# Kernel tuning notes

Measured on AMD Instinct MI355X. Metric: run time of the kernel, lower is better.

## Reference

```python
import jax, jax.numpy as jnp
import numpy as np

N_NODES = 50000
N_EDGES = 800000
F_IN, F_HID, F_OUT = 128, 256, 64


def setup_inputs() -> dict:
    key = jax.random.key(0)
    ks = jax.random.split(key, 8)
    return {
        "x": jax.random.normal(ks[0], (N_NODES, F_IN), dtype=jnp.float32),
        "edge_index": jax.random.randint(ks[1], (2, N_EDGES), 0, N_NODES, dtype=jnp.int32),
        "W_l1": jax.random.normal(ks[2], (F_IN, F_HID), dtype=jnp.float32) * (1.0 / np.sqrt(F_IN)),
        "W_r1": jax.random.normal(ks[3], (F_IN, F_HID), dtype=jnp.float32) * (1.0 / np.sqrt(F_IN)),
        "b1": jnp.zeros((F_HID,), dtype=jnp.float32),
        "W_l2": jax.random.normal(ks[4], (F_HID, F_OUT), dtype=jnp.float32) * (1.0 / np.sqrt(F_HID)),
        "W_r2": jax.random.normal(ks[5], (F_HID, F_OUT), dtype=jnp.float32) * (1.0 / np.sqrt(F_HID)),
        "b2": jnp.zeros((F_OUT,), dtype=jnp.float32),
    }


def _sage_conv(x, src, dst, W_l, W_r, b):
    # PyG SAGEConv, mean aggregation:
    #   out = mean_{j in N(i)} x_j @ W_l + b + x_i @ W_r
    n = x.shape[0]
    msgs = x[src]                                              # [E, F] gather
    agg_sum = jax.ops.segment_sum(msgs, dst, num_segments=n)   # [N, F] scatter-add
    deg = jax.ops.segment_sum(jnp.ones_like(dst, dtype=x.dtype), dst, num_segments=n)
    agg = agg_sum / jnp.maximum(deg, 1.0)[:, None]             # isolated nodes -> 0
    return agg @ W_l + x @ W_r + b


def reference(x, edge_index, W_l1, W_r1, b1, W_l2, W_r2, b2):
    src, dst = edge_index[0], edge_index[1]
    # layer 1 + relu (dropout is identity in eval mode)
    h = jax.nn.relu(_sage_conv(x, src, dst, W_l1, W_r1, b1))
    # layer 2, multi_class=False -> sigmoid
    out = jax.nn.sigmoid(_sage_conv(h, src, dst, W_l2, W_r2, b2))
    return out
```

## Files before the change

kernel.cpp:

```cpp
#include <hip/hip_runtime.h>
#include <cstdint>
#include <cstddef>


#define N_NODES 50000
#define N_EDGES 800000
#define F_IN 128
#define F_HID 256
#define F_OUT 64
#define CAP 48
#define BINW 128

#define NBIN ((N_NODES + BINW - 1) / BINW)
#define EPB 4096
#define NBLK_A ((N_EDGES + EPB - 1) / EPB)
#define CHUNK 32

#define PREP_TOTAL (N_NODES * 64 + 256 * 256 + 128 * 256)
#define NBLK_PREP ((PREP_TOTAL + 255) / 256)

typedef __attribute__((ext_vector_type(8))) short bf16x8;
typedef __attribute__((ext_vector_type(4))) float f32x4;
typedef __attribute__((ext_vector_type(2))) float f32x2;

__device__ inline unsigned short f2bf(float f) {
    unsigned int u = __float_as_uint(f);
    u += 0x7fffu + ((u >> 16) & 1u);
    return (unsigned short)(u >> 16);
}
__device__ inline unsigned int pack_bf2(float lo, float hi) {
    return (unsigned int)f2bf(lo) | ((unsigned int)f2bf(hi) << 16);
}
__device__ inline float bf_lo(unsigned int u) { return __uint_as_float(u << 16); }
__device__ inline float bf_hi(unsigned int u) { return __uint_as_float(u & 0xffff0000u); }

__device__ inline void gload16(const short* g, short* l) {
    __builtin_amdgcn_global_load_lds(
        (const __attribute__((address_space(1))) void*)g,
        (__attribute__((address_space(3))) void*)l, 16, 0, 0);
}

__global__ __launch_bounds__(256) void binprep_kernel(
    const int* __restrict__ src, const int* __restrict__ dst, int* __restrict__ blkbincnt,
    unsigned int* __restrict__ chunks, const float* __restrict__ x,
    const float* __restrict__ Wl1, const float* __restrict__ Wr1, const float* __restrict__ Wl2,
    const float* __restrict__ Wr2, unsigned int* __restrict__ xbf,
    unsigned short* __restrict__ xq16, short* __restrict__ Bt1, short* __restrict__ Bt2) {
    __shared__ unsigned int ls[NBIN * CHUNK];
    __shared__ int hist[NBIN];
    const int bid = blockIdx.x;
    const int tid = threadIdx.x;
    if (bid < NBLK_A) {
        for (int i = tid; i < NBIN; i += 256) hist[i] = 0;
        __syncthreads();
        const int base = bid * EPB;
        const int nloc = min(EPB, N_EDGES - base);
        for (int j = tid; j < nloc; j += 256) {
            int e = base + j;
            int d = dst[e];
            int s = src[e];
            int bin = d >> 7;
            int p = atomicAdd(&hist[bin], 1);
            if (p < CHUNK)
                ls[bin * CHUNK + p] = ((unsigned int)(d & (BINW - 1)) << 16) | (unsigned int)s;
        }
        __syncthreads();
        for (int i = tid; i < NBIN; i += 256) blkbincnt[bid * NBIN + i] = hist[i];
        unsigned int* outp = &chunks[(size_t)bid * NBIN * CHUNK];
        for (int idx = tid; idx < NBIN * CHUNK; idx += 256) {
            int bin = idx >> 5, i = idx & 31;
            if (i < min(hist[bin], CHUNK)) outp[idx] = ls[idx];
        }
        return;
    }
    int i = (bid - NBLK_A) * 256 + tid;
    if (i < N_NODES * 64) {
        int row = i >> 6, c = i & 63;
        float2 f = *reinterpret_cast<const float2*>(&x[(size_t)row * F_IN + 2 * c]);
        xbf[(size_t)row * 64 + c] = pack_bf2(f.x, f.y);
        xq16[(size_t)row * 64 + c] =
            (unsigned short)(__builtin_amdgcn_cvt_pk_fp8_f32(f.x, f.y, 0, false) & 0xffff);
        return;
    }
    i -= N_NODES * 64;
    if (i < 256 * 256) {
        int k = i >> 8, n = i & 255;
        float v = (k < 128) ? Wl1[k * 256 + n] : Wr1[(k - 128) * 256 + n];
        Bt1[n * 256 + k] = (short)f2bf(v);
        return;
    }
    i -= 256 * 256;
    if (i < 128 * 256) {
        int k = i >> 7, n = i & 127;
        float v = (n < 64) ? Wl2[k * 64 + n] : Wr2[k * 64 + (n - 64)];
        Bt2[n * 256 + k] = (short)f2bf(v);
    }
}

__global__ __launch_bounds__(1024) void bpart_agg_kernel(const unsigned int* __restrict__ chunks,
                                                         const int* __restrict__ blkbincnt,
                                                         int* __restrict__ cnt,
                                                         unsigned short* __restrict__ slots,
                                                         const unsigned int* __restrict__ xq,
                                                         unsigned int* __restrict__ aggx) {
    __shared__ int cur[BINW];
    __shared__ unsigned short ls[BINW * CAP];
    __shared__ int ccnt[NBLK_A];
    const int bin = blockIdx.x;
    const int tid = threadIdx.x;
    if (tid < BINW) cur[tid] = 0;
    for (int i = tid; i < NBLK_A; i += 1024) ccnt[i] = min(blkbincnt[i * NBIN + bin], CHUNK);
    __syncthreads();
    for (int idx = tid; idx < NBLK_A * CHUNK; idx += 1024) {
        int blk = idx >> 5, i = idx & 31;
        if (i < ccnt[blk]) {
            unsigned int pk = chunks[((size_t)blk * NBIN + bin) * CHUNK + i];
            int dl = pk >> 16;
            int p = atomicAdd(&cur[dl], 1);
            if (p < CAP) ls[dl * CAP + p] = (unsigned short)(pk & 0xffffu);
        }
    }
    __syncthreads();
    if (tid < BINW) {
        int node = bin * BINW + tid;
        if (node < N_NODES) cnt[node] = cur[tid];
    }
    const uint4* lsv = reinterpret_cast<const uint4*>(ls);
    uint4* gv = reinterpret_cast<uint4*>(&slots[(size_t)bin * BINW * CAP]);
    for (int i = tid; i < BINW * 6; i += 1024) {
        int row = i / 6;
        if (bin * BINW + row < N_NODES) gv[i] = lsv[i];
    }
    const int nl = tid >> 5;
    const int t = tid & 31;
    for (int nb = 0; nb < BINW / 32; ++nb) {
        const int local = nb * 32 + nl;
        const int node = bin * BINW + local;
        if (node >= N_NODES) continue;
        const int deg = cur[local];
        const int n = min(deg, CAP);
        const unsigned short* sl = &ls[local * CAP];
        float a0 = 0.f, a1 = 0.f, a2 = 0.f, a3 = 0.f;
        int j = 0;
        for (; j + 16 <= n; j += 16) {
            uint4 sv0 = *reinterpret_cast<const uint4*>(&sl[j]);
            uint4 sv1 = *reinterpret_cast<const uint4*>(&sl[j + 8]);
            int s[16];
            s[0] = sv0.x & 0xffff; s[1] = sv0.x >> 16;
            s[2] = sv0.y & 0xffff; s[3] = sv0.y >> 16;
            s[4] = sv0.z & 0xffff; s[5] = sv0.z >> 16;
            s[6] = sv0.w & 0xffff; s[7] = sv0.w >> 16;
            s[8] = sv1.x & 0xffff; s[9] = sv1.x >> 16;
            s[10] = sv1.y & 0xffff; s[11] = sv1.y >> 16;
            s[12] = sv1.z & 0xffff; s[13] = sv1.z >> 16;
            s[14] = sv1.w & 0xffff; s[15] = sv1.w >> 16;
            unsigned int u[16];
#pragma unroll
            for (int q = 0; q < 16; ++q) u[q] = xq[(size_t)s[q] * 32 + t];
#pragma unroll
            for (int q = 0; q < 16; ++q) {
                f32x2 lo = __builtin_amdgcn_cvt_pk_f32_fp8((int)u[q], false);
                f32x2 hi = __builtin_amdgcn_cvt_pk_f32_fp8((int)u[q], true);
                a0 += lo.x; a1 += lo.y; a2 += hi.x; a3 += hi.y;
            }
        }
        for (; j + 8 <= n; j += 8) {
            uint4 sv = *reinterpret_cast<const uint4*>(&sl[j]);
            int s[8];
            s[0] = sv.x & 0xffff; s[1] = sv.x >> 16;
            s[2] = sv.y & 0xffff; s[3] = sv.y >> 16;
            s[4] = sv.z & 0xffff; s[5] = sv.z >> 16;
            s[6] = sv.w & 0xffff; s[7] = sv.w >> 16;
            unsigned int u[8];
#pragma unroll
            for (int q = 0; q < 8; ++q) u[q] = xq[(size_t)s[q] * 32 + t];
#pragma unroll
            for (int q = 0; q < 8; ++q) {
                f32x2 lo = __builtin_amdgcn_cvt_pk_f32_fp8((int)u[q], false);
                f32x2 hi = __builtin_amdgcn_cvt_pk_f32_fp8((int)u[q], true);
                a0 += lo.x; a1 += lo.y; a2 += hi.x; a3 += hi.y;
            }
        }
        for (; j < n; ++j) {
            unsigned int u = xq[(size_t)sl[j] * 32 + t];
            f32x2 lo = __builtin_amdgcn_cvt_pk_f32_fp8((int)u, false);
            f32x2 hi = __builtin_amdgcn_cvt_pk_f32_fp8((int)u, true);
            a0 += lo.x; a1 += lo.y; a2 += hi.x; a3 += hi.y;
        }
        float scale = (deg > 0) ? 1.0f / (float)deg : 0.0f;
        uint2 o;
        o.x = pack_bf2(a0 * scale, a1 * scale);
        o.y = pack_bf2(a2 * scale, a3 * scale);
        *reinterpret_cast<uint2*>(&aggx[(size_t)node * 64 + t * 2]) = o;
    }
}

#define LDH 264
__global__ __launch_bounds__(256) void gemm_fused_kernel(const short* __restrict__ Aagg,
                                                         const short* __restrict__ Aself,
                                                         const short* __restrict__ Bt1,
                                                         const short* __restrict__ Bt2,
                                                         const float* __restrict__ b1,
                                                         unsigned char* __restrict__ grq,
                                                         short* __restrict__ grR) {
    __shared__ short smem[64 * LDH + 128 * 64];
    short* As = smem;
    short* Bs1 = smem + 64 * 64;
    short* Hs = smem;
    short* Bs2 = smem + 64 * LDH;

    const int tid = threadIdx.x;
    const int lane = tid & 63;
    const int wave = tid >> 6;
    const int quad = lane >> 4;
    const int l16 = lane & 15;
    const int m0 = blockIdx.x * 64;
    const int M = N_NODES;

    const int srow = lane >> 3;
    const int sswz = (lane & 7) ^ srow;

    f32x4 acc[4][4];
#pragma unroll
    for (int i = 0; i < 4; ++i)
#pragma unroll
        for (int j = 0; j < 4; ++j) acc[i][j] = (f32x4)(0.0f);

    const int wn1 = wave * 64;

    for (int k0 = 0; k0 < 256; k0 += 64) {
        const short* Asrc = (k0 < 128) ? Aagg : Aself;
        const int kbase = k0 & 127;
#pragma unroll
        for (int j = 0; j < 2; ++j) {
            int i = wave * 2 + j;
            int row = i * 8 + srow;
            int gm = m0 + row;
            gm = (gm < M) ? gm : (M - 1);
            gload16(Asrc + (size_t)gm * 128 + kbase + (sswz << 3), As + i * 512);
        }
#pragma unroll
        for (int j = 0; j < 8; ++j) {
            int i = wave + j * 4;
            int row = i * 8 + srow;
            gload16(Bt1 + (size_t)row * 256 + k0 + (sswz << 3), Bs1 + i * 512);
        }
        __syncthreads();
#pragma unroll
        for (int kk = 0; kk < 64; kk += 32) {
            const int sw = (((kk >> 3) + quad) ^ (l16 & 7)) << 3;
            bf16x8 af[4], bfr[4];
#pragma unroll
            for (int mi = 0; mi < 4; ++mi)
                af[mi] = *reinterpret_cast<const bf16x8*>(&As[(mi * 16 + l16) * 64 + sw]);
#pragma unroll
            for (int ni = 0; ni < 4; ++ni)
                bfr[ni] = *reinterpret_cast<const bf16x8*>(
                    &Bs1[(wn1 + ni * 16 + l16) * 64 + sw]);
#pragma unroll
            for (int mi = 0; mi < 4; ++mi)
#pragma unroll
                for (int ni = 0; ni < 4; ++ni)
                    acc[mi][ni] = __builtin_amdgcn_mfma_f32_16x16x32_bf16(af[mi], bfr[ni],
                                                                          acc[mi][ni], 0, 0, 0);
        }
        __syncthreads();
    }

    float biasv[4];
#pragma unroll
    for (int ni = 0; ni < 4; ++ni) biasv[ni] = b1[wn1 + ni * 16 + l16];
#pragma unroll
    for (int mi = 0; mi < 4; ++mi)
#pragma unroll
        for (int reg = 0; reg < 4; ++reg) {
            int row = mi * 16 + quad * 4 + reg;
#pragma unroll
            for (int ni = 0; ni < 4; ++ni) {
                float v = fmaxf(acc[mi][ni][reg] + biasv[ni], 0.0f);
                Hs[row * LDH + wn1 + ni * 16 + l16] = (short)f2bf(v);
            }
        }
    __syncthreads();

    f32x4 acc2[2][4];
#pragma unroll
    for (int i = 0; i < 2; ++i)
#pragma unroll
        for (int j = 0; j < 4; ++j) acc2[i][j] = (f32x4)(0.0f);

    const int wm2 = (wave >> 1) * 32;
    const int wn2 = (wave & 1) * 64;

    for (int k0 = 0; k0 < 256; k0 += 64) {
#pragma unroll
        for (int j = 0; j < 4; ++j) {
            int i = wave + j * 4;
            int row = i * 8 + srow;
            gload16(Bt2 + (size_t)row * 256 + k0 + (sswz << 3), Bs2 + i * 512);
        }
        __syncthreads();
#pragma unroll
        for (int kk = 0; kk < 64; kk += 32) {
            const int sw = (((kk >> 3) + quad) ^ (l16 & 7)) << 3;
            bf16x8 af[2], bfr[4];
#pragma unroll
            for (int mi = 0; mi < 2; ++mi)
                af[mi] = *reinterpret_cast<const bf16x8*>(
                    &Hs[(wm2 + mi * 16 + l16) * LDH + k0 + kk + quad * 8]);
#pragma unroll
            for (int ni = 0; ni < 4; ++ni)
                bfr[ni] = *reinterpret_cast<const bf16x8*>(
                    &Bs2[(wn2 + ni * 16 + l16) * 64 + sw]);
#pragma unroll
            for (int mi = 0; mi < 2; ++mi)
#pragma unroll
                for (int ni = 0; ni < 4; ++ni)
                    acc2[mi][ni] = __builtin_amdgcn_mfma_f32_16x16x32_bf16(af[mi], bfr[ni],
                                                                           acc2[mi][ni], 0, 0, 0);
        }
        __syncthreads();
    }

#pragma unroll
    for (int mi = 0; mi < 2; ++mi)
#pragma unroll
        for (int reg = 0; reg < 4; ++reg) {
            int gm = m0 + wm2 + mi * 16 + quad * 4 + reg;
            if (gm >= M) continue;
#pragma unroll
            for (int ni = 0; ni < 4; ++ni) {
                int gn = wn2 + ni * 16 + l16;
                float v = acc2[mi][ni][reg];
                if (gn < 64) {
                    grq[(size_t)gm * 64 + gn] =
                        (unsigned char)(__builtin_amdgcn_cvt_pk_fp8_f32(v, v, 0, false) & 0xff);
                } else {
                    grR[(size_t)gm * 64 + (gn - 64)] = (short)f2bf(v);
                }
            }
        }
}

__global__ __launch_bounds__(256) void final_kernel(const unsigned int* __restrict__ grq,
                                                    const unsigned int* __restrict__ grRu,
                                                    const int* __restrict__ cnt,
                                                    const unsigned short* __restrict__ slots,
                                                    const float* __restrict__ b2,
                                                    float* __restrict__ out) {
    const int node = blockIdx.x * 16 + (threadIdx.x >> 4);
    const int t = threadIdx.x & 15;
    if (node >= N_NODES) return;
    const int deg = cnt[node];
    const int n = min(deg, CAP);
    const unsigned short* sl = &slots[(size_t)node * CAP];
    float a0 = 0.f, a1 = 0.f, a2 = 0.f, a3 = 0.f;
    int j = 0;
    for (; j + 16 <= n; j += 16) {
        uint4 sv0 = *reinterpret_cast<const uint4*>(&sl[j]);
        uint4 sv1 = *reinterpret_cast<const uint4*>(&sl[j + 8]);
        int s[16];
        s[0] = sv0.x & 0xffff; s[1] = sv0.x >> 16;
        s[2] = sv0.y & 0xffff; s[3] = sv0.y >> 16;
        s[4] = sv0.z & 0xffff; s[5] = sv0.z >> 16;
        s[6] = sv0.w & 0xffff; s[7] = sv0.w >> 16;
        s[8] = sv1.x & 0xffff; s[9] = sv1.x >> 16;
        s[10] = sv1.y & 0xffff; s[11] = sv1.y >> 16;
        s[12] = sv1.z & 0xffff; s[13] = sv1.z >> 16;
        s[14] = sv1.w & 0xffff; s[15] = sv1.w >> 16;
        unsigned int u[16];
#pragma unroll
        for (int q = 0; q < 16; ++q) u[q] = grq[(size_t)s[q] * 16 + t];
#pragma unroll
        for (int q = 0; q < 16; ++q) {
            f32x2 lo = __builtin_amdgcn_cvt_pk_f32_fp8((int)u[q], false);
            f32x2 hi = __builtin_amdgcn_cvt_pk_f32_fp8((int)u[q], true);
            a0 += lo.x; a1 += lo.y; a2 += hi.x; a3 += hi.y;
        }
    }
    for (; j + 8 <= n; j += 8) {
        uint4 sv = *reinterpret_cast<const uint4*>(&sl[j]);
        int s[8];
        s[0] = sv.x & 0xffff; s[1] = sv.x >> 16;
        s[2] = sv.y & 0xffff; s[3] = sv.y >> 16;
        s[4] = sv.z & 0xffff; s[5] = sv.z >> 16;
        s[6] = sv.w & 0xffff; s[7] = sv.w >> 16;
        unsigned int u[8];
#pragma unroll
        for (int q = 0; q < 8; ++q) u[q] = grq[(size_t)s[q] * 16 + t];
#pragma unroll
        for (int q = 0; q < 8; ++q) {
            f32x2 lo = __builtin_amdgcn_cvt_pk_f32_fp8((int)u[q], false);
            f32x2 hi = __builtin_amdgcn_cvt_pk_f32_fp8((int)u[q], true);
            a0 += lo.x; a1 += lo.y; a2 += hi.x; a3 += hi.y;
        }
    }
    for (; j < n; ++j) {
        unsigned int u = grq[(size_t)sl[j] * 16 + t];
        f32x2 lo = __builtin_amdgcn_cvt_pk_f32_fp8((int)u, false);
        f32x2 hi = __builtin_amdgcn_cvt_pk_f32_fp8((int)u, true);
        a0 += lo.x; a1 += lo.y; a2 += hi.x; a3 += hi.y;
    }
    float scale = (deg > 0) ? 1.0f / (float)deg : 0.0f;
    uint2 r = *reinterpret_cast<const uint2*>(&grRu[(size_t)node * 32 + t * 2]);
    float4 bv = *reinterpret_cast<const float4*>(&b2[t * 4]);
    float v0 = a0 * scale + bf_lo(r.x) + bv.x;
    float v1 = a1 * scale + bf_hi(r.x) + bv.y;
    float v2 = a2 * scale + bf_lo(r.y) + bv.z;
    float v3 = a3 * scale + bf_hi(r.y) + bv.w;
    float4 o;
    o.x = 1.0f / (1.0f + __expf(-v0));
    o.y = 1.0f / (1.0f + __expf(-v1));
    o.z = 1.0f / (1.0f + __expf(-v2));
    o.w = 1.0f / (1.0f + __expf(-v3));
    *reinterpret_cast<float4*>(&out[(size_t)node * 64 + t * 4]) = o;
}


extern "C" void kernel_launch(void* const* d_in, const int* in_sizes, int n_in,
                              void* d_out, int out_size, void* d_ws, size_t ws_size,
                              hipStream_t stream) {
    const float* x   = (const float*)d_in[0];
    const int* ei    = (const int*)d_in[1];
    const float* Wl1 = (const float*)d_in[2];
    const float* Wr1 = (const float*)d_in[3];
    const float* b1  = (const float*)d_in[4];
    const float* Wl2 = (const float*)d_in[5];
    const float* Wr2 = (const float*)d_in[6];
    const float* b2  = (const float*)d_in[7];
    float* out       = (float*)d_out;

    const int* src = ei;
    const int* dst = ei + N_EDGES;

    char* p = (char*)d_ws;
    auto alloc = [&](size_t bytes) {
        char* r = p;
        p += (bytes + 255) & ~(size_t)255;
        return (void*)r;
    };
    int* cnt              = (int*)alloc((size_t)N_NODES * 4);
    unsigned short* slots = (unsigned short*)alloc((size_t)NBIN * BINW * CAP * 2);
    int* blkbincnt        = (int*)alloc((size_t)NBLK_A * NBIN * 4);
    unsigned int* chunks  = (unsigned int*)alloc((size_t)NBLK_A * NBIN * CHUNK * 4);
    unsigned int* xbf     = (unsigned int*)alloc((size_t)N_NODES * 64 * 4);
    unsigned short* xq16  = (unsigned short*)alloc((size_t)N_NODES * 64 * 2);
    unsigned int* aggx    = (unsigned int*)alloc((size_t)N_NODES * 64 * 4);
    unsigned char* grq    = (unsigned char*)alloc((size_t)N_NODES * 64);
    short* grR            = (short*)alloc((size_t)N_NODES * 64 * 2);
    short* Bt1            = (short*)alloc((size_t)256 * 256 * 2);
    short* Bt2            = (short*)alloc((size_t)128 * 256 * 2);
    (void)ws_size;

    binprep_kernel<<<NBLK_A + NBLK_PREP, 256, 0, stream>>>(src, dst, blkbincnt, chunks, x, Wl1,
                                                           Wr1, Wl2, Wr2, xbf, xq16, Bt1, Bt2);
    bpart_agg_kernel<<<NBIN, 1024, 0, stream>>>(chunks, blkbincnt, cnt, slots,
                                                (const unsigned int*)xq16, aggx);

    gemm_fused_kernel<<<(N_NODES + 63) / 64, 256, 0, stream>>>(
        (const short*)aggx, (const short*)xbf, Bt1, Bt2, b1, grq, grR);

    final_kernel<<<(N_NODES + 15) / 16, 256, 0, stream>>>((const unsigned int*)grq,
                                                          (const unsigned int*)grR, cnt, slots,
                                                          b2, out);
}
```

Measured before the change: 166.3 us.

## Merge GEMM and final aggregation into one cooperative persistent kernel

Combines the fused two-layer GEMM kernel and the final gather/sigmoid kernel into one persistent cooperative kernel. Blocks loop over GEMM tiles, hit a grid-wide barrier, then loop over node chunks for the layer-2 aggregation. This removes one kernel launch and its inter-kernel gap. In exchange it adds a grid sync and a persistent grid capped by occupancy (launch bounds 256,3), which may lower parallelism and tail efficiency compared with the original oversubscribed grids.

```diff
diff --git a/kernel.cpp b/kernel.cpp
--- a/kernel.cpp
+++ b/kernel.cpp
@@ -1,6 +1,9 @@
 #include <hip/hip_runtime.h>
+#include <hip/hip_cooperative_groups.h>
 #include <cstdint>
 #include <cstddef>
+
+namespace cg = cooperative_groups;
 
 
 #define N_NODES 50000
@@ -18,6 +21,9 @@
 
 #define PREP_TOTAL (N_NODES * 64 + 256 * 256 + 128 * 256)
 #define NBLK_PREP ((PREP_TOTAL + 255) / 256)
+
+#define NTILE ((N_NODES + 63) / 64)
+#define NCHUNK ((N_NODES + 15) / 16)
 
 typedef __attribute__((ext_vector_type(8))) short bf16x8;
 typedef __attribute__((ext_vector_type(4))) float f32x4;
@@ -196,13 +202,13 @@
 }
 
 #define LDH 264
-__global__ __launch_bounds__(256) void gemm_fused_kernel(const short* __restrict__ Aagg,
-                                                         const short* __restrict__ Aself,
-                                                         const short* __restrict__ Bt1,
-                                                         const short* __restrict__ Bt2,
-                                                         const float* __restrict__ b1,
-                                                         unsigned char* __restrict__ grq,
-                                                         short* __restrict__ grR) {
+__global__ __launch_bounds__(256, 3) void gemm_final_kernel(
+    const short* __restrict__ Aagg, const short* __restrict__ Aself,
+    const short* __restrict__ Bt1, const short* __restrict__ Bt2,
+    const float* __restrict__ b1, unsigned char* __restrict__ grq,
+    short* __restrict__ grR, const int* __restrict__ cnt,
+    const unsigned short* __restrict__ slots, const float* __restrict__ b2,
+    float* __restrict__ out) {
     __shared__ short smem[64 * LDH + 128 * 64];
     short* As = smem;
     short* Bs1 = smem + 64 * 64;
@@ -214,206 +220,210 @@
     const int wave = tid >> 6;
     const int quad = lane >> 4;
     const int l16 = lane & 15;
-    const int m0 = blockIdx.x * 64;
     const int M = N_NODES;
 
     const int srow = lane >> 3;
     const int sswz = (lane & 7) ^ srow;
 
-    f32x4 acc[4][4];
-#pragma unroll
-    for (int i = 0; i < 4; ++i)
-#pragma unroll
-        for (int j = 0; j < 4; ++j) acc[i][j] = (f32x4)(0.0f);
-
-    const int wn1 = wave * 64;
-
-    for (int k0 = 0; k0 < 256; k0 += 64) {
-        const short* Asrc = (k0 < 128) ? Aagg : Aself;
-        const int kbase = k0 & 127;
-#pragma unroll
-        for (int j = 0; j < 2; ++j) {
-            int i = wave * 2 + j;
-            int row = i * 8 + srow;
-            int gm = m0 + row;
-            gm = (gm < M) ? gm : (M - 1);
-            gload16(Asrc + (size_t)gm * 128 + kbase + (sswz << 3), As + i * 512);
-        }
-#pragma unroll
-        for (int j = 0; j < 8; ++j) {
-            int i = wave + j * 4;
-            int row = i * 8 + srow;
-            gload16(Bt1 + (size_t)row * 256 + k0 + (sswz << 3), Bs1 + i * 512);
-        }
+    for (int tile = blockIdx.x; tile < NTILE; tile += gridDim.x) {
+        const int m0 = tile * 64;
+
+        f32x4 acc[4][4];
+#pragma unroll
+        for (int i = 0; i < 4; ++i)
+#pragma unroll
+            for (int j = 0; j < 4; ++j) acc[i][j] = (f32x4)(0.0f);
+
+        const int wn1 = wave * 64;
+
+        for (int k0 = 0; k0 < 256; k0 += 64) {
+            const short* Asrc = (k0 < 128) ? Aagg : Aself;
+            const int kbase = k0 & 127;
+#pragma unroll
+            for (int j = 0; j < 2; ++j) {
+                int i = wave * 2 + j;
+                int row = i * 8 + srow;
+                int gm = m0 + row;
+                gm = (gm < M) ? gm : (M - 1);
+                gload16(Asrc + (size_t)gm * 128 + kbase + (sswz << 3), As + i * 512);
+            }
+#pragma unroll
+            for (int j = 0; j < 8; ++j) {
+                int i = wave + j * 4;
+                int row = i * 8 + srow;
+                gload16(Bt1 + (size_t)row * 256 + k0 + (sswz << 3), Bs1 + i * 512);
+            }
+            __syncthreads();
+#pragma unroll
+            for (int kk = 0; kk < 64; kk += 32) {
+                const int sw = (((kk >> 3) + quad) ^ (l16 & 7)) << 3;
+                bf16x8 af[4], bfr[4];
+#pragma unroll
+                for (int mi = 0; mi < 4; ++mi)
+                    af[mi] = *reinterpret_cast<const bf16x8*>(&As[(mi * 16 + l16) * 64 + sw]);
+#pragma unroll
+                for (int ni = 0; ni < 4; ++ni)
+                    bfr[ni] = *reinterpret_cast<const bf16x8*>(
+                        &Bs1[(wn1 + ni * 16 + l16) * 64 + sw]);
+#pragma unroll
+                for (int mi = 0; mi < 4; ++mi)
+#pragma unroll
+                    for (int ni = 0; ni < 4; ++ni)
+                        acc[mi][ni] = __builtin_amdgcn_mfma_f32_16x16x32_bf16(
+                            af[mi], bfr[ni], acc[mi][ni], 0, 0, 0);
+            }
+            __syncthreads();
+        }
+
+        float biasv[4];
+#pragma unroll
+        for (int ni = 0; ni < 4; ++ni) biasv[ni] = b1[wn1 + ni * 16 + l16];
+#pragma unroll
+        for (int mi = 0; mi < 4; ++mi)
+#pragma unroll
+            for (int reg = 0; reg < 4; ++reg) {
+                int row = mi * 16 + quad * 4 + reg;
+#pragma unroll
+                for (int ni = 0; ni < 4; ++ni) {
+                    float v = fmaxf(acc[mi][ni][reg] + biasv[ni], 0.0f);
+                    Hs[row * LDH + wn1 + ni * 16 + l16] = (short)f2bf(v);
+                }
+            }
         __syncthreads();
-#pragma unroll
-        for (int kk = 0; kk < 64; kk += 32) {
-            const int sw = (((kk >> 3) + quad) ^ (l16 & 7)) << 3;
-            bf16x8 af[4], bfr[4];
-#pragma unroll
-            for (int mi = 0; mi < 4; ++mi)
-                af[mi] = *reinterpret_cast<const bf16x8*>(&As[(mi * 16 + l16) * 64 + sw]);
-#pragma unroll
-            for (int ni = 0; ni < 4; ++ni)
-                bfr[ni] = *reinterpret_cast<const bf16x8*>(
-                    &Bs1[(wn1 + ni * 16 + l16) * 64 + sw]);
-#pragma unroll
-            for (int mi = 0; mi < 4; ++mi)
+
+        f32x4 acc2[2][4];
+#pragma unroll
+        for (int i = 0; i < 2; ++i)
+#pragma unroll
+            for (int j = 0; j < 4; ++j) acc2[i][j] = (f32x4)(0.0f);
+
+        const int wm2 = (wave >> 1) * 32;
+        const int wn2 = (wave & 1) * 64;
+
+        for (int k0 = 0; k0 < 256; k0 += 64) {
+#pragma unroll
+            for (int j = 0; j < 4; ++j) {
+                int i = wave + j * 4;
+                int row = i * 8 + srow;
+                gload16(Bt2 + (size_t)row * 256 + k0 + (sswz << 3), Bs2 + i * 512);
+            }
+            __syncthreads();
+#pragma unroll
+            for (int kk = 0; kk < 64; kk += 32) {
+                const int sw = (((kk >> 3) + quad) ^ (l16 & 7)) << 3;
+                bf16x8 af[2], bfr[4];
+#pragma unroll
+                for (int mi = 0; mi < 2; ++mi)
+                    af[mi] = *reinterpret_cast<const bf16x8*>(
+                        &Hs[(wm2 + mi * 16 + l16) * LDH + k0 + kk + quad * 8]);
 #pragma unroll
                 for (int ni = 0; ni < 4; ++ni)
-                    acc[mi][ni] = __builtin_amdgcn_mfma_f32_16x16x32_bf16(af[mi], bfr[ni],
-                                                                          acc[mi][ni], 0, 0, 0);
-        }
+                    bfr[ni] = *reinterpret_cast<const bf16x8*>(
+                        &Bs2[(wn2 + ni * 16 + l16) * 64 + sw]);
+#pragma unroll
+                for (int mi = 0; mi < 2; ++mi)
+#pragma unroll
+                    for (int ni = 0; ni < 4; ++ni)
+                        acc2[mi][ni] = __builtin_amdgcn_mfma_f32_16x16x32_bf16(
+                            af[mi], bfr[ni], acc2[mi][ni], 0, 0, 0);
+            }
+            __syncthreads();
+        }
+
+#pragma unroll
+        for (int mi = 0; mi < 2; ++mi)
+#pragma unroll
+            for (int reg = 0; reg < 4; ++reg) {
+                int gm = m0 + wm2 + mi * 16 + quad * 4 + reg;
+                if (gm >= M) continue;
+#pragma unroll
+                for (int ni = 0; ni < 4; ++ni) {
+                    int gn = wn2 + ni * 16 + l16;
+                    float v = acc2[mi][ni][reg];
+                    if (gn < 64) {
+                        grq[(size_t)gm * 64 + gn] =
+                            (unsigned char)(__builtin_amdgcn_cvt_pk_fp8_f32(v, v, 0, false) & 0xff);
+                    } else {
+                        grR[(size_t)gm * 64 + (gn - 64)] = (short)f2bf(v);
+                    }
+                }
+            }
         __syncthreads();
     }
 
-    float biasv[4];
-#pragma unroll
-    for (int ni = 0; ni < 4; ++ni) biasv[ni] = b1[wn1 + ni * 16 + l16];
-#pragma unroll
-    for (int mi = 0; mi < 4; ++mi)
-#pragma unroll
-        for (int reg = 0; reg < 4; ++reg) {
-            int row = mi * 16 + quad * 4 + reg;
-#pragma unroll
-            for (int ni = 0; ni < 4; ++ni) {
-                float v = fmaxf(acc[mi][ni][reg] + biasv[ni], 0.0f);
-                Hs[row * LDH + wn1 + ni * 16 + l16] = (short)f2bf(v);
-            }
-        }
-    __syncthreads();
-
-    f32x4 acc2[2][4];
-#pragma unroll
-    for (int i = 0; i < 2; ++i)
-#pragma unroll
-        for (int j = 0; j < 4; ++j) acc2[i][j] = (f32x4)(0.0f);
-
-    const int wm2 = (wave >> 1) * 32;
-    const int wn2 = (wave & 1) * 64;
-
-    for (int k0 = 0; k0 < 256; k0 += 64) {
-#pragma unroll
-        for (int j = 0; j < 4; ++j) {
-            int i = wave + j * 4;
-            int row = i * 8 + srow;
-            gload16(Bt2 + (size_t)row * 256 + k0 + (sswz << 3), Bs2 + i * 512);
-        }
-        __syncthreads();
-#pragma unroll
-        for (int kk = 0; kk < 64; kk += 32) {
-            const int sw = (((kk >> 3) + quad) ^ (l16 & 7)) << 3;
-            bf16x8 af[2], bfr[4];
-#pragma unroll
-            for (int mi = 0; mi < 2; ++mi)
-                af[mi] = *reinterpret_cast<const bf16x8*>(
-                    &Hs[(wm2 + mi * 16 + l16) * LDH + k0 + kk + quad * 8]);
-#pragma unroll
-            for (int ni = 0; ni < 4; ++ni)
-                bfr[ni] = *reinterpret_cast<const bf16x8*>(
-                    &Bs2[(wn2 + ni * 16 + l16) * 64 + sw]);
-#pragma unroll
-            for (int mi = 0; mi < 2; ++mi)
-#pragma unroll
-                for (int ni = 0; ni < 4; ++ni)
-                    acc2[mi][ni] = __builtin_amdgcn_mfma_f32_16x16x32_bf16(af[mi], bfr[ni],
-                                                                           acc2[mi][ni], 0, 0, 0);
-        }
-        __syncthreads();
-    }
-
-#pragma unroll
-    for (int mi = 0; mi < 2; ++mi)
-#pragma unroll
-        for (int reg = 0; reg < 4; ++reg) {
-            int gm = m0 + wm2 + mi * 16 + quad * 4 + reg;
-            if (gm >= M) continue;
-#pragma unroll
-            for (int ni = 0; ni < 4; ++ni) {
-                int gn = wn2 + ni * 16 + l16;
-                float v = acc2[mi][ni][reg];
-                if (gn < 64) {
-                    grq[(size_t)gm * 64 + gn] =
-                        (unsigned char)(__builtin_amdgcn_cvt_pk_fp8_f32(v, v, 0, false) & 0xff);
-                } else {
-                    grR[(size_t)gm * 64 + (gn - 64)] = (short)f2bf(v);
-                }
-            }
-        }
-}
-
-__global__ __launch_bounds__(256) void final_kernel(const unsigned int* __restrict__ grq,
-                                                    const unsigned int* __restrict__ grRu,
-                                                    const int* __restrict__ cnt,
-                                                    const unsigned short* __restrict__ slots,
-                                                    const float* __restrict__ b2,
-                                                    float* __restrict__ out) {
-    const int node = blockIdx.x * 16 + (threadIdx.x >> 4);
-    const int t = threadIdx.x & 15;
-    if (node >= N_NODES) return;
-    const int deg = cnt[node];
-    const int n = min(deg, CAP);
-    const unsigned short* sl = &slots[(size_t)node * CAP];
-    float a0 = 0.f, a1 = 0.f, a2 = 0.f, a3 = 0.f;
-    int j = 0;
-    for (; j + 16 <= n; j += 16) {
-        uint4 sv0 = *reinterpret_cast<const uint4*>(&sl[j]);
-        uint4 sv1 = *reinterpret_cast<const uint4*>(&sl[j + 8]);
-        int s[16];
-        s[0] = sv0.x & 0xffff; s[1] = sv0.x >> 16;
-        s[2] = sv0.y & 0xffff; s[3] = sv0.y >> 16;
-        s[4] = sv0.z & 0xffff; s[5] = sv0.z >> 16;
-        s[6] = sv0.w & 0xffff; s[7] = sv0.w >> 16;
-        s[8] = sv1.x & 0xffff; s[9] = sv1.x >> 16;
-        s[10] = sv1.y & 0xffff; s[11] = sv1.y >> 16;
-        s[12] = sv1.z & 0xffff; s[13] = sv1.z >> 16;
-        s[14] = sv1.w & 0xffff; s[15] = sv1.w >> 16;
-        unsigned int u[16];
-#pragma unroll
-        for (int q = 0; q < 16; ++q) u[q] = grq[(size_t)s[q] * 16 + t];
-#pragma unroll
-        for (int q = 0; q < 16; ++q) {
-            f32x2 lo = __builtin_amdgcn_cvt_pk_f32_fp8((int)u[q], false);
-            f32x2 hi = __builtin_amdgcn_cvt_pk_f32_fp8((int)u[q], true);
+    __threadfence();
+    cg::this_grid().sync();
+
+    const unsigned int* grqU = reinterpret_cast<const unsigned int*>(grq);
+    const unsigned int* grRu = reinterpret_cast<const unsigned int*>(grR);
+    for (int c = blockIdx.x; c < NCHUNK; c += gridDim.x) {
+        const int node = c * 16 + (threadIdx.x >> 4);
+        const int t = threadIdx.x & 15;
+        if (node >= N_NODES) continue;
+        const int deg = cnt[node];
+        const int n = min(deg, CAP);
+        const unsigned short* sl = &slots[(size_t)node * CAP];
+        float a0 = 0.f, a1 = 0.f, a2 = 0.f, a3 = 0.f;
+        int j = 0;
+        for (; j + 16 <= n; j += 16) {
+            uint4 sv0 = *reinterpret_cast<const uint4*>(&sl[j]);
+            uint4 sv1 = *reinterpret_cast<const uint4*>(&sl[j + 8]);
+            int s[16];
+            s[0] = sv0.x & 0xffff; s[1] = sv0.x >> 16;
+            s[2] = sv0.y & 0xffff; s[3] = sv0.y >> 16;
+            s[4] = sv0.z & 0xffff; s[5] = sv0.z >> 16;
+            s[6] = sv0.w & 0xffff; s[7] = sv0.w >> 16;
+            s[8] = sv1.x & 0xffff; s[9] = sv1.x >> 16;
+            s[10] = sv1.y & 0xffff; s[11] = sv1.y >> 16;
+            s[12] = sv1.z & 0xffff; s[13] = sv1.z >> 16;
+            s[14] = sv1.w & 0xffff; s[15] = sv1.w >> 16;
+            unsigned int u[16];
+#pragma unroll
+            for (int q = 0; q < 16; ++q) u[q] = grqU[(size_t)s[q] * 16 + t];
+#pragma unroll
+            for (int q = 0; q < 16; ++q) {
+                f32x2 lo = __builtin_amdgcn_cvt_pk_f32_fp8((int)u[q], false);
+                f32x2 hi = __builtin_amdgcn_cvt_pk_f32_fp8((int)u[q], true);
+                a0 += lo.x; a1 += lo.y; a2 += hi.x; a3 += hi.y;
+            }
+        }
+        for (; j + 8 <= n; j += 8) {
+            uint4 sv = *reinterpret_cast<const uint4*>(&sl[j]);
+            int s[8];
+            s[0] = sv.x & 0xffff; s[1] = sv.x >> 16;
+            s[2] = sv.y & 0xffff; s[3] = sv.y >> 16;
+            s[4] = sv.z & 0xffff; s[5] = sv.z >> 16;
+            s[6] = sv.w & 0xffff; s[7] = sv.w >> 16;
+            unsigned int u[8];
+#pragma unroll
+            for (int q = 0; q < 8; ++q) u[q] = grqU[(size_t)s[q] * 16 + t];
+#pragma unroll
+            for (int q = 0; q < 8; ++q) {
+                f32x2 lo = __builtin_amdgcn_cvt_pk_f32_fp8((int)u[q], false);
+                f32x2 hi = __builtin_amdgcn_cvt_pk_f32_fp8((int)u[q], true);
+                a0 += lo.x; a1 += lo.y; a2 += hi.x; a3 += hi.y;
+            }
+        }
+        for (; j < n; ++j) {
+            unsigned int u = grqU[(size_t)sl[j] * 16 + t];
+            f32x2 lo = __builtin_amdgcn_cvt_pk_f32_fp8((int)u, false);
+            f32x2 hi = __builtin_amdgcn_cvt_pk_f32_fp8((int)u, true);
             a0 += lo.x; a1 += lo.y; a2 += hi.x; a3 += hi.y;
         }
-    }
-    for (; j + 8 <= n; j += 8) {
-        uint4 sv = *reinterpret_cast<const uint4*>(&sl[j]);
-        int s[8];
-        s[0] = sv.x & 0xffff; s[1] = sv.x >> 16;
-        s[2] = sv.y & 0xffff; s[3] = sv.y >> 16;
-        s[4] = sv.z & 0xffff; s[5] = sv.z >> 16;
-        s[6] = sv.w & 0xffff; s[7] = sv.w >> 16;
-        unsigned int u[8];
-#pragma unroll
-        for (int q = 0; q < 8; ++q) u[q] = grq[(size_t)s[q] * 16 + t];
-#pragma unroll
-        for (int q = 0; q < 8; ++q) {
-            f32x2 lo = __builtin_amdgcn_cvt_pk_f32_fp8((int)u[q], false);
-            f32x2 hi = __builtin_amdgcn_cvt_pk_f32_fp8((int)u[q], true);
-            a0 += lo.x; a1 += lo.y; a2 += hi.x; a3 += hi.y;
-        }
-    }
-    for (; j < n; ++j) {
-        unsigned int u = grq[(size_t)sl[j] * 16 + t];
-        f32x2 lo = __builtin_amdgcn_cvt_pk_f32_fp8((int)u, false);
-        f32x2 hi = __builtin_amdgcn_cvt_pk_f32_fp8((int)u, true);
-        a0 += lo.x; a1 += lo.y; a2 += hi.x; a3 += hi.y;
-    }
-    float scale = (deg > 0) ? 1.0f / (float)deg : 0.0f;
-    uint2 r = *reinterpret_cast<const uint2*>(&grRu[(size_t)node * 32 + t * 2]);
-    float4 bv = *reinterpret_cast<const float4*>(&b2[t * 4]);
-    float v0 = a0 * scale + bf_lo(r.x) + bv.x;
-    float v1 = a1 * scale + bf_hi(r.x) + bv.y;
-    float v2 = a2 * scale + bf_lo(r.y) + bv.z;
-    float v3 = a3 * scale + bf_hi(r.y) + bv.w;
-    float4 o;
-    o.x = 1.0f / (1.0f + __expf(-v0));
-    o.y = 1.0f / (1.0f + __expf(-v1));
-    o.z = 1.0f / (1.0f + __expf(-v2));
-    o.w = 1.0f / (1.0f + __expf(-v3));
-    *reinterpret_cast<float4*>(&out[(size_t)node * 64 + t * 4]) = o;
+        float scale = (deg > 0) ? 1.0f / (float)deg : 0.0f;
+        uint2 r = *reinterpret_cast<const uint2*>(&grRu[(size_t)node * 32 + t * 2]);
+        float4 bv = *reinterpret_cast<const float4*>(&b2[t * 4]);
+        float v0 = a0 * scale + bf_lo(r.x) + bv.x;
+        float v1 = a1 * scale + bf_hi(r.x) + bv.y;
+        float v2 = a2 * scale + bf_lo(r.y) + bv.z;
+        float v3 = a3 * scale + bf_hi(r.y) + bv.w;
+        float4 o;
+        o.x = 1.0f / (1.0f + __expf(-v0));
+        o.y = 1.0f / (1.0f + __expf(-v1));
+        o.z = 1.0f / (1.0f + __expf(-v2));
+        o.w = 1.0f / (1.0f + __expf(-v3));
+        *reinterpret_cast<float4*>(&out[(size_t)node * 64 + t * 4]) = o;
+    }
 }
 
 
@@ -457,10 +467,26 @@
     bpart_agg_kernel<<<NBIN, 1024, 0, stream>>>(chunks, blkbincnt, cnt, slots,
                                                 (const unsigned int*)xq16, aggx);
 
-    gemm_fused_kernel<<<(N_NODES + 63) / 64, 256, 0, stream>>>(
-        (const short*)aggx, (const short*)xbf, Bt1, Bt2, b1, grq, grR);
-
-    final_kernel<<<(N_NODES + 15) / 16, 256, 0, stream>>>((const unsigned int*)grq,
-                                                          (const unsigned int*)grR, cnt, slots,
-                                                          b2, out);
-}
+    int nb = 0;
+    hipOccupancyMaxActiveBlocksPerMultiprocessor(&nb, gemm_final_kernel, 256, 0);
+    if (nb < 1) nb = 1;
+    int grid = nb * 256;
+    if (grid > NTILE) grid = NTILE;
+
+    const short* Aagg_p  = (const short*)aggx;
+    const short* Aself_p = (const short*)xbf;
+    const short* Bt1_p   = Bt1;
+    const short* Bt2_p   = Bt2;
+    const float* b1_p    = b1;
+    unsigned char* grq_p = grq;
+    short* grR_p         = grR;
+    const int* cnt_p     = cnt;
+    const unsigned short* slots_p = slots;
+    const float* b2_p    = b2;
+    float* out_p         = out;
+    void* kargs[] = {(void*)&Aagg_p, (void*)&Aself_p, (void*)&Bt1_p, (void*)&Bt2_p,
+                     (void*)&b1_p,   (void*)&grq_p,   (void*)&grR_p, (void*)&cnt_p,
+                     (void*)&slots_p, (void*)&b2_p,   (void*)&out_p};
+    hipLaunchCooperativeKernel((void*)gemm_final_kernel, dim3(grid), dim3(256),
+                               kargs, 0, stream);
+}
```

New measurement: 329.9 us. 98.4% more time.

## Split fp8 node features into two half-width tables for two-pass gather

Applied to the files above, without the earlier changes.

The fp8-quantized input features are stored as two separate 64-byte-per-row tables instead of one 128-byte table. The layer-1 aggregation gathers each half in its own pass, with 16 threads per node instead of 32. The aim is to shrink the random-gather working set to fit in cache better (3.2MB per half). The cost is reading the neighbor index lists twice and issuing more, narrower gather loads.

```diff
diff --git a/kernel.cpp b/kernel.cpp
--- a/kernel.cpp
+++ b/kernel.cpp
@@ -45,7 +45,8 @@
     unsigned int* __restrict__ chunks, const float* __restrict__ x,
     const float* __restrict__ Wl1, const float* __restrict__ Wr1, const float* __restrict__ Wl2,
     const float* __restrict__ Wr2, unsigned int* __restrict__ xbf,
-    unsigned short* __restrict__ xq16, short* __restrict__ Bt1, short* __restrict__ Bt2) {
+    unsigned short* __restrict__ xqA, unsigned short* __restrict__ xqB,
+    short* __restrict__ Bt1, short* __restrict__ Bt2) {
     __shared__ unsigned int ls[NBIN * CHUNK];
     __shared__ int hist[NBIN];
     const int bid = blockIdx.x;
@@ -78,8 +79,10 @@
         int row = i >> 6, c = i & 63;
         float2 f = *reinterpret_cast<const float2*>(&x[(size_t)row * F_IN + 2 * c]);
         xbf[(size_t)row * 64 + c] = pack_bf2(f.x, f.y);
-        xq16[(size_t)row * 64 + c] =
+        unsigned short v8 =
             (unsigned short)(__builtin_amdgcn_cvt_pk_fp8_f32(f.x, f.y, 0, false) & 0xffff);
+        if (c < 32) xqA[(size_t)row * 32 + c] = v8;
+        else        xqB[(size_t)row * 32 + (c - 32)] = v8;
         return;
     }
     i -= N_NODES * 64;
@@ -101,7 +104,8 @@
                                                          const int* __restrict__ blkbincnt,
                                                          int* __restrict__ cnt,
                                                          unsigned short* __restrict__ slots,
-                                                         const unsigned int* __restrict__ xq,
+                                                         const unsigned int* __restrict__ xqA,
+                                                         const unsigned int* __restrict__ xqB,
                                                          unsigned int* __restrict__ aggx) {
     __shared__ int cur[BINW];
     __shared__ unsigned short ls[BINW * CAP];
@@ -131,67 +135,70 @@
         int row = i / 6;
         if (bin * BINW + row < N_NODES) gv[i] = lsv[i];
     }
-    const int nl = tid >> 5;
-    const int t = tid & 31;
-    for (int nb = 0; nb < BINW / 32; ++nb) {
-        const int local = nb * 32 + nl;
-        const int node = bin * BINW + local;
-        if (node >= N_NODES) continue;
-        const int deg = cur[local];
-        const int n = min(deg, CAP);
-        const unsigned short* sl = &ls[local * CAP];
-        float a0 = 0.f, a1 = 0.f, a2 = 0.f, a3 = 0.f;
-        int j = 0;
-        for (; j + 16 <= n; j += 16) {
-            uint4 sv0 = *reinterpret_cast<const uint4*>(&sl[j]);
-            uint4 sv1 = *reinterpret_cast<const uint4*>(&sl[j + 8]);
-            int s[16];
-            s[0] = sv0.x & 0xffff; s[1] = sv0.x >> 16;
-            s[2] = sv0.y & 0xffff; s[3] = sv0.y >> 16;
-            s[4] = sv0.z & 0xffff; s[5] = sv0.z >> 16;
-            s[6] = sv0.w & 0xffff; s[7] = sv0.w >> 16;
-            s[8] = sv1.x & 0xffff; s[9] = sv1.x >> 16;
-            s[10] = sv1.y & 0xffff; s[11] = sv1.y >> 16;
-            s[12] = sv1.z & 0xffff; s[13] = sv1.z >> 16;
-            s[14] = sv1.w & 0xffff; s[15] = sv1.w >> 16;
-            unsigned int u[16];
-#pragma unroll
-            for (int q = 0; q < 16; ++q) u[q] = xq[(size_t)s[q] * 32 + t];
-#pragma unroll
-            for (int q = 0; q < 16; ++q) {
-                f32x2 lo = __builtin_amdgcn_cvt_pk_f32_fp8((int)u[q], false);
-                f32x2 hi = __builtin_amdgcn_cvt_pk_f32_fp8((int)u[q], true);
+    const int grp = tid >> 4;
+    const int t = tid & 15;
+    for (int pass = 0; pass < 2; ++pass) {
+        const unsigned int* xqh = pass ? xqB : xqA;
+        for (int nb = 0; nb < BINW / 64; ++nb) {
+            const int local = nb * 64 + grp;
+            const int node = bin * BINW + local;
+            if (node >= N_NODES) continue;
+            const int deg = cur[local];
+            const int n = min(deg, CAP);
+            const unsigned short* sl = &ls[local * CAP];
+            float a0 = 0.f, a1 = 0.f, a2 = 0.f, a3 = 0.f;
+            int j = 0;
+            for (; j + 16 <= n; j += 16) {
+                uint4 sv0 = *reinterpret_cast<const uint4*>(&sl[j]);
+                uint4 sv1 = *reinterpret_cast<const uint4*>(&sl[j + 8]);
+                int s[16];
+                s[0] = sv0.x & 0xffff; s[1] = sv0.x >> 16;
+                s[2] = sv0.y & 0xffff; s[3] = sv0.y >> 16;
+                s[4] = sv0.z & 0xffff; s[5] = sv0.z >> 16;
+                s[6] = sv0.w & 0xffff; s[7] = sv0.w >> 16;
+                s[8] = sv1.x & 0xffff; s[9] = sv1.x >> 16;
+                s[10] = sv1.y & 0xffff; s[11] = sv1.y >> 16;
+                s[12] = sv1.z & 0xffff; s[13] = sv1.z >> 16;
+                s[14] = sv1.w & 0xffff; s[15] = sv1.w >> 16;
+                unsigned int u[16];
+#pragma unroll
+                for (int q = 0; q < 16; ++q) u[q] = xqh[(size_t)s[q] * 16 + t];
+#pragma unroll
+                for (int q = 0; q < 16; ++q) {
+                    f32x2 lo = __builtin_amdgcn_cvt_pk_f32_fp8((int)u[q], false);
+                    f32x2 hi = __builtin_amdgcn_cvt_pk_f32_fp8((int)u[q], true);
+                    a0 += lo.x; a1 += lo.y; a2 += hi.x; a3 += hi.y;
+                }
+            }
+            for (; j + 8 <= n; j += 8) {
+                uint4 sv = *reinterpret_cast<const uint4*>(&sl[j]);
+                int s[8];
+                s[0] = sv.x & 0xffff; s[1] = sv.x >> 16;
+                s[2] = sv.y & 0xffff; s[3] = sv.y >> 16;
+                s[4] = sv.z & 0xffff; s[5] = sv.z >> 16;
+                s[6] = sv.w & 0xffff; s[7] = sv.w >> 16;
+                unsigned int u[8];
+#pragma unroll
+                for (int q = 0; q < 8; ++q) u[q] = xqh[(size_t)s[q] * 16 + t];
+#pragma unroll
+                for (int q = 0; q < 8; ++q) {
+                    f32x2 lo = __builtin_amdgcn_cvt_pk_f32_fp8((int)u[q], false);
+                    f32x2 hi = __builtin_amdgcn_cvt_pk_f32_fp8((int)u[q], true);
+                    a0 += lo.x; a1 += lo.y; a2 += hi.x; a3 += hi.y;
+                }
+            }
+            for (; j < n; ++j) {
+                unsigned int u = xqh[(size_t)sl[j] * 16 + t];
+                f32x2 lo = __builtin_amdgcn_cvt_pk_f32_fp8((int)u, false);
+                f32x2 hi = __builtin_amdgcn_cvt_pk_f32_fp8((int)u, true);
                 a0 += lo.x; a1 += lo.y; a2 += hi.x; a3 += hi.y;
             }
-        }
-        for (; j + 8 <= n; j += 8) {
-            uint4 sv = *reinterpret_cast<const uint4*>(&sl[j]);
-            int s[8];
-            s[0] = sv.x & 0xffff; s[1] = sv.x >> 16;
-            s[2] = sv.y & 0xffff; s[3] = sv.y >> 16;
-            s[4] = sv.z & 0xffff; s[5] = sv.z >> 16;
-            s[6] = sv.w & 0xffff; s[7] = sv.w >> 16;
-            unsigned int u[8];
-#pragma unroll
-            for (int q = 0; q < 8; ++q) u[q] = xq[(size_t)s[q] * 32 + t];
-#pragma unroll
-            for (int q = 0; q < 8; ++q) {
-                f32x2 lo = __builtin_amdgcn_cvt_pk_f32_fp8((int)u[q], false);
-                f32x2 hi = __builtin_amdgcn_cvt_pk_f32_fp8((int)u[q], true);
-                a0 += lo.x; a1 += lo.y; a2 += hi.x; a3 += hi.y;
-            }
-        }
-        for (; j < n; ++j) {
-            unsigned int u = xq[(size_t)sl[j] * 32 + t];
-            f32x2 lo = __builtin_amdgcn_cvt_pk_f32_fp8((int)u, false);
-            f32x2 hi = __builtin_amdgcn_cvt_pk_f32_fp8((int)u, true);
-            a0 += lo.x; a1 += lo.y; a2 += hi.x; a3 += hi.y;
-        }
-        float scale = (deg > 0) ? 1.0f / (float)deg : 0.0f;
-        uint2 o;
-        o.x = pack_bf2(a0 * scale, a1 * scale);
-        o.y = pack_bf2(a2 * scale, a3 * scale);
-        *reinterpret_cast<uint2*>(&aggx[(size_t)node * 64 + t * 2]) = o;
+            float scale = (deg > 0) ? 1.0f / (float)deg : 0.0f;
+            uint2 o;
+            o.x = pack_bf2(a0 * scale, a1 * scale);
+            o.y = pack_bf2(a2 * scale, a3 * scale);
+            *reinterpret_cast<uint2*>(&aggx[(size_t)node * 64 + pass * 32 + t * 2]) = o;
+        }
     }
 }
 
@@ -444,7 +451,8 @@
     int* blkbincnt        = (int*)alloc((size_t)NBLK_A * NBIN * 4);
     unsigned int* chunks  = (unsigned int*)alloc((size_t)NBLK_A * NBIN * CHUNK * 4);
     unsigned int* xbf     = (unsigned int*)alloc((size_t)N_NODES * 64 * 4);
-    unsigned short* xq16  = (unsigned short*)alloc((size_t)N_NODES * 64 * 2);
+    unsigned short* xqA   = (unsigned short*)alloc((size_t)N_NODES * 32 * 2);
+    unsigned short* xqB   = (unsigned short*)alloc((size_t)N_NODES * 32 * 2);
     unsigned int* aggx    = (unsigned int*)alloc((size_t)N_NODES * 64 * 4);
     unsigned char* grq    = (unsigned char*)alloc((size_t)N_NODES * 64);
     short* grR            = (short*)alloc((size_t)N_NODES * 64 * 2);
@@ -453,9 +461,11 @@
     (void)ws_size;
 
     binprep_kernel<<<NBLK_A + NBLK_PREP, 256, 0, stream>>>(src, dst, blkbincnt, chunks, x, Wl1,
-                                                           Wr1, Wl2, Wr2, xbf, xq16, Bt1, Bt2);
+                                                           Wr1, Wl2, Wr2, xbf, xqA, xqB, Bt1,
+                                                           Bt2);
     bpart_agg_kernel<<<NBIN, 1024, 0, stream>>>(chunks, blkbincnt, cnt, slots,
-                                                (const unsigned int*)xq16, aggx);
+                                                (const unsigned int*)xqA,
+                                                (const unsigned int*)xqB, aggx);
 
     gemm_fused_kernel<<<(N_NODES + 63) / 64, 256, 0, stream>>>(
         (const short*)aggx, (const short*)xbf, Bt1, Bt2, b1, grq, grR);
```

Measured after the change: 168.8 us. No clear change (+1.5%).
